# Kernel optimization log

Measured on AMD Instinct MI355X. Metric: run time of the kernel, lower is better.

## Reference

```python
import jax, jax.numpy as jnp
import numpy as np

BLOCK = (4, 4, 4)
NUM_HEADS = 8


def setup_inputs() -> dict:
    key = jax.random.key(0)
    ks = jax.random.split(key, 5)
    C = 128
    return {
        "x": jax.random.normal(ks[0], (2, C, 32, 62, 62), dtype=jnp.float32),
        "qkv_w": jax.random.normal(ks[1], (3 * C, C), dtype=jnp.float32) * 0.02,
        "qkv_b": jax.random.normal(ks[2], (3 * C,), dtype=jnp.float32) * 0.02,
        "conv_w": jax.random.normal(ks[3], (C, C, 1, 1, 1), dtype=jnp.float32) * 0.02,
        "conv_b": jax.random.normal(ks[4], (C,), dtype=jnp.float32) * 0.02,
    }


def reference(x, qkv_w, qkv_b, conv_w, conv_b):
    b0, b1, b2 = BLOCK
    heads = NUM_HEADS
    B, C, D, H0, W0 = x.shape
    pad_r = (-W0) % b2
    pad_b = (-H0) % b1
    x = jnp.pad(x, ((0, 0), (0, 0), (0, 0), (0, pad_b), (0, pad_r)))
    H, W = H0 + pad_b, W0 + pad_r
    d, h, w = D // b0, H // b1, W // b2
    hd = C // heads
    scale = hd ** (-0.5)
    T = b0 * b1 * b2  # tokens per 3D window
    nw = d * h * w    # number of windows

    # partition into windows: (B, nw, T, C)
    xw = x.reshape(B, C, d, b0, h, b1, w, b2).transpose(0, 2, 4, 6, 3, 5, 7, 1)
    xw = xw.reshape(B, nw, T, C)

    qkv = xw @ qkv_w.T + qkv_b  # (B, nw, T, 3C)
    qkv = qkv.reshape(B, nw, T, 3, heads, hd).transpose(3, 0, 1, 4, 2, 5)
    q, k, v = qkv[0], qkv[1], qkv[2]  # (B, nw, heads, T, hd)

    attn = jnp.einsum('bnhtc,bnhsc->bnhts', q, k) * scale

    if pad_r > 0 or pad_b > 0:
        mask = jnp.zeros((H, W), dtype=attn.dtype)
        if pad_b > 0:
            mask = mask.at[-pad_b:, :].set(1.0)
        if pad_r > 0:
            mask = mask.at[:, -pad_r:].set(1.0)
        # (h*w, b1*b2) per-2D-window pad flags
        mask = mask.reshape(h, b1, w, b2).transpose(0, 2, 1, 3).reshape(h * w, b1 * b2)
        am = mask[:, None, :] - mask[:, :, None]  # (h*w, b1*b2, b1*b2)
        am = jnp.where(am != 0, jnp.asarray(-1000.0, attn.dtype), jnp.asarray(0.0, attn.dtype))
        # tile over depth windows and depth tokens (matches torch .repeat)
        am = jnp.tile(am, (d, b0, b0))  # (nw, T, T)
        attn = attn + am[None, :, None, :, :]

    attn = jax.nn.softmax(attn, axis=-1)
    o = jnp.einsum('bnhts,bnhsc->bnhtc', attn, v)  # (B, nw, heads, T, hd)

    o = o.reshape(B, d, h, w, heads, b0, b1, b2, hd)
    o = o.transpose(0, 4, 8, 1, 5, 2, 6, 3, 7).reshape(B, C, D, H, W)
    o = o[:, :, :, :H0, :W0]

    # 1x1x1 Conv3d == channel mixing
    out = jnp.einsum('bcdhw,oc->bodhw', o, conv_w[:, :, 0, 0, 0])
    out = out + conv_b[None, :, None, None, None]
    return out
```

## Files before the change

### kernel.cpp

```cpp
#include <hip/hip_runtime.h>

typedef _Float16 f16x8 __attribute__((ext_vector_type(8)));
typedef _Float16 f16x4 __attribute__((ext_vector_type(4)));
typedef __fp16   fp16x2 __attribute__((ext_vector_type(2)));
typedef float    f32x4 __attribute__((ext_vector_type(4)));
typedef unsigned int u32x2 __attribute__((ext_vector_type(2)));

__device__ __forceinline__ f32x4 mfma32(f16x8 a, f16x8 b, f32x4 c) {
  return __builtin_amdgcn_mfma_f32_16x16x32_f16(a, b, c, 0, 0, 0);
}
__device__ __forceinline__ f32x4 mfma16(f16x4 a, f16x4 b, f32x4 c) {
#if __has_builtin(__builtin_amdgcn_mfma_f32_16x16x16f16)
  return __builtin_amdgcn_mfma_f32_16x16x16f16(a, b, c, 0, 0, 0);
#else
  f32x4 d;
  asm volatile("v_mfma_f32_16x16x16_f16 %0, %1, %2, %3"
               : "=v"(d) : "v"(a), "v"(b), "v"(c));
  return d;
#endif
}

__device__ __forceinline__ unsigned pk2(float a, float b) {
  union { fp16x2 h; unsigned u; } cv;
  cv.h = __builtin_amdgcn_cvt_pkrtz(a, b);
  return cv.u;
}

#define TR_READ(dst, addr, OFF) \
  asm volatile("ds_read_b64_tr_b16 %0, %1 offset:" OFF \
               : "=v"(dst) : "v"(addr) : "memory")

__global__ void cvt_weights(const float* __restrict__ qw, const float* __restrict__ cw,
                            _Float16* __restrict__ wq, _Float16* __restrict__ wc) {
  const int i = blockIdx.x * 256 + threadIdx.x;
  if (i < 384 * 128) wq[i] = (_Float16)qw[i];
  if (i < 128 * 128) wc[i] = (_Float16)cw[i];
}

__global__ void __launch_bounds__(256, 4)
win_attn(const float* __restrict__ xg, const _Float16* __restrict__ wq,
         const float* __restrict__ qbias, const _Float16* __restrict__ wc,
         const float* __restrict__ cb, float* __restrict__ outg)
{
  __shared__ char xsm[16384];
  __shared__ char wsm[4][6144];

  const int tid  = threadIdx.x;
  const int lane = tid & 63;
  const int wv   = tid >> 6;
  const int l15  = lane & 15;
  const int g    = lane >> 4;

  const int raw = blockIdx.x;
  const int wid = ((raw & 7) << 9) | (raw >> 3);
  const int ww = wid & 15, hh = (wid >> 4) & 15, dd = (wid >> 8) & 7, bb = wid >> 11;

  const f32x4 fz = {0.f, 0.f, 0.f, 0.f};

  {
    const int m4 = lane & 3, q4 = lane >> 2;
    const int i0 = q4 >> 2, i1 = q4 & 3;
    const int z = dd * 4 + i0, y = hh * 4 + i1;
    const bool yv   = (y < 62);
    const bool full = (ww < 15);
    float va[8][4];
#pragma unroll
    for (int it = 0; it < 8; ++it) {
      const int c = wv * 32 + it * 4 + m4;
      const float* src = xg + (((size_t)(bb * 128 + c) * 32 + (size_t)z) * 3844
                               + (size_t)(y * 62 + ww * 4));
      float a0 = 0.f, a1 = 0.f, a2 = 0.f, a3 = 0.f;
      if (yv) {
        const float2 lo = *reinterpret_cast<const float2*>(src);
        a0 = lo.x; a1 = lo.y;
        if (full) {
          const float2 hi = *reinterpret_cast<const float2*>(src + 2);
          a2 = hi.x; a3 = hi.y;
        }
      }
      va[it][0] = a0; va[it][1] = a1; va[it][2] = a2; va[it][3] = a3;
    }
#pragma unroll
    for (int it = 0; it < 8; ++it) {
      float v0 = va[it][0], v1 = va[it][1], v2 = va[it][2], v3 = va[it][3];
      float t0 = __shfl_xor((m4 & 1) ? v0 : v1, 1);
      float t1 = __shfl_xor((m4 & 1) ? v2 : v3, 1);
      if (m4 & 1) { v0 = t0; v2 = t1; } else { v1 = t0; v3 = t1; }
      float t2 = __shfl_xor((m4 & 2) ? v0 : v2, 2);
      float t3 = __shfl_xor((m4 & 2) ? v1 : v3, 2);
      if (m4 & 2) { v0 = t2; v1 = t3; } else { v2 = t2; v3 = t3; }
      f16x4 pk; pk[0] = (_Float16)v0; pk[1] = (_Float16)v1;
                pk[2] = (_Float16)v2; pk[3] = (_Float16)v3;
      const int c0 = wv * 32 + it * 4;
      *reinterpret_cast<f16x4*>(xsm + ((lane * 256 + 2 * c0) ^ ((lane & 15) << 4))) = pk;
    }
  }
  __syncthreads();

  char* sb = wsm[wv];
  const unsigned sb32 = (unsigned)(unsigned long long)sb;
  const unsigned trb  = sb32 + 8u * (unsigned)lane;
  const int vswz = (l15 & 7) << 4;

  unsigned long long pm = 0ull;
  if (hh == 15) pm |= 0xFF00FF00FF00FF00ull;
  if (ww == 15) pm |= 0xCCCCCCCCCCCCCCCCull;

  const float LOG2E = 1.4426950408889634f;
  const int swzA = l15 << 4;

  unsigned opk0[4][2], opk1[4][2];

#pragma unroll
  for (int hp = 0; hp < 2; ++hp) {
    __builtin_amdgcn_sched_barrier(0);
#pragma unroll
    for (int co = 0; co < 3; ++co) {
      f32x4 acc[4] = {fz, fz, fz, fz};
      const int col = co * 128 + wv * 32 + hp * 16 + l15;
#pragma unroll
      for (int kk = 0; kk < 4; ++kk) {
        const f16x8 bfr = *reinterpret_cast<const f16x8*>(wq + col * 128 + kk * 32 + g * 8);
#pragma unroll
        for (int ri = 0; ri < 4; ++ri) {
          const f16x8 a = *reinterpret_cast<const f16x8*>(
              xsm + (ri * 16 + l15) * 256 + ((kk * 64 + g * 16) ^ swzA));
          acc[ri] = mfma32(a, bfr, acc[ri]);
        }
      }
      const float bias = qbias[col];
      const float sc = (co == 0) ? 0.25f : 1.0f;
#pragma unroll
      for (int ri = 0; ri < 4; ++ri)
#pragma unroll
        for (int r = 0; r < 4; ++r) acc[ri][r] = (acc[ri][r] + bias) * sc;

      if (co == 2) {
#pragma unroll
        for (int ri = 0; ri < 4; ++ri) {
          const int s0 = ri * 16 + g * 4;
          *reinterpret_cast<unsigned*>(sb + 4096 + l15 * 128 + ((2 * s0) ^ vswz))
              = pk2(acc[ri][0], acc[ri][1]);
          *reinterpret_cast<unsigned*>(sb + 4096 + l15 * 128 + ((2 * (s0 + 2)) ^ vswz))
              = pk2(acc[ri][2], acc[ri][3]);
        }
      } else {
        const int base = (co == 0) ? 2048 : 0;
#pragma unroll
        for (int ri = 0; ri < 4; ++ri) {
          const int off = ri * 512 + l15 * 32 + g * 8;
          u32x2 w;
          w[0] = pk2(acc[ri][0], acc[ri][1]);
          w[1] = pk2(acc[ri][2], acc[ri][3]);
          *reinterpret_cast<u32x2*>(sb + base + off) = w;
        }
      }
      __builtin_amdgcn_sched_barrier(0);
    }
    asm volatile("s_waitcnt lgkmcnt(0)" ::: "memory");

    f16x4 ka[4], qa[4];
    TR_READ(ka[0], trb, "0");
    TR_READ(ka[1], trb, "512");
    TR_READ(ka[2], trb, "1024");
    TR_READ(ka[3], trb, "1536");
    TR_READ(qa[0], trb, "2048");
    TR_READ(qa[1], trb, "2560");
    TR_READ(qa[2], trb, "3072");
    TR_READ(qa[3], trb, "3584");
    f16x8 av0, av1;
    av0 = *reinterpret_cast<const f16x8*>(sb + 4096 + l15 * 128 + ((g * 16) ^ vswz));
    av1 = *reinterpret_cast<const f16x8*>(sb + 4096 + l15 * 128 + ((64 + g * 16) ^ vswz));
    asm volatile("s_waitcnt lgkmcnt(0)" ::: "memory");
    __builtin_amdgcn_sched_barrier(0);

    f32x4 oa0, oa1;
#pragma unroll
    for (int tjp = 0; tjp < 2; ++tjp) {
      const int tj0 = 2 * tjp, tj1 = 2 * tjp + 1;
      f32x4 st2[4][2];
#pragma unroll
      for (int si = 0; si < 4; ++si) {
        st2[si][0] = mfma16(ka[si], qa[tj0], fz);
        st2[si][1] = mfma16(ka[si], qa[tj1], fz);
      }

      if (pm) {
#pragma unroll
        for (int tjc = 0; tjc < 2; ++tjc) {
          const int t = (2 * tjp + tjc) * 16 + l15;
          const unsigned ft = (unsigned)(pm >> t) & 1u;
#pragma unroll
          for (int si = 0; si < 4; ++si)
#pragma unroll
            for (int r = 0; r < 4; ++r) {
              const int s = si * 16 + g * 4 + r;
              const unsigned fs = (unsigned)(pm >> s) & 1u;
              if (fs != ft) st2[si][tjc][r] -= 1000.f;
            }
        }
      }

#pragma unroll
      for (int tjc = 0; tjc < 2; ++tjc) {
        float mx = st2[0][tjc][0];
#pragma unroll
        for (int si = 0; si < 4; ++si)
#pragma unroll
          for (int r = 0; r < 4; ++r) mx = fmaxf(mx, st2[si][tjc][r]);
        mx = fmaxf(mx, __shfl_xor(mx, 16));
        mx = fmaxf(mx, __shfl_xor(mx, 32));
        float sum = 0.f;
#pragma unroll
        for (int si = 0; si < 4; ++si)
#pragma unroll
          for (int r = 0; r < 4; ++r) {
            const float e = __builtin_amdgcn_exp2f((st2[si][tjc][r] - mx) * LOG2E);
            st2[si][tjc][r] = e; sum += e;
          }
        sum += __shfl_xor(sum, 16);
        sum += __shfl_xor(sum, 32);
        const float inv = __builtin_amdgcn_rcpf(sum);
#pragma unroll
        for (int si = 0; si < 4; ++si)
#pragma unroll
          for (int r = 0; r < 4; ++r) st2[si][tjc][r] *= inv;
      }

#pragma unroll
      for (int tjc = 0; tjc < 2; ++tjc) {
        const int tl = tjc * 16 + l15;
#pragma unroll
        for (int si = 0; si < 4; ++si) {
          u32x2 w;
          w[0] = pk2(st2[si][tjc][0], st2[si][tjc][1]);
          w[1] = pk2(st2[si][tjc][2], st2[si][tjc][3]);
          *reinterpret_cast<u32x2*>(sb + tl * 128 + ((si * 32 + g * 8) ^ vswz)) = w;
        }
      }
      asm volatile("s_waitcnt lgkmcnt(0)" ::: "memory");

      oa0 = fz; oa1 = fz;
      {
        const f16x8 pa00 = *reinterpret_cast<const f16x8*>(
            sb + l15 * 128 + ((g * 16) ^ vswz));
        const f16x8 pa10 = *reinterpret_cast<const f16x8*>(
            sb + (16 + l15) * 128 + ((g * 16) ^ vswz));
        oa0 = mfma32(av0, pa00, oa0);
        oa1 = mfma32(av0, pa10, oa1);
        const f16x8 pa01 = *reinterpret_cast<const f16x8*>(
            sb + l15 * 128 + ((64 + g * 16) ^ vswz));
        const f16x8 pa11 = *reinterpret_cast<const f16x8*>(
            sb + (16 + l15) * 128 + ((64 + g * 16) ^ vswz));
        oa0 = mfma32(av1, pa01, oa0);
        oa1 = mfma32(av1, pa11, oa1);
      }

      if (hp == 0) {
        opk0[tj0][0] = pk2(oa0[0], oa0[1]); opk0[tj0][1] = pk2(oa0[2], oa0[3]);
        opk0[tj1][0] = pk2(oa1[0], oa1[1]); opk0[tj1][1] = pk2(oa1[2], oa1[3]);
      } else {
        opk1[tj0][0] = pk2(oa0[0], oa0[1]); opk1[tj0][1] = pk2(oa0[2], oa0[3]);
        opk1[tj1][0] = pk2(oa1[0], oa1[1]); opk1[tj1][1] = pk2(oa1[2], oa1[3]);
      }
      __builtin_amdgcn_sched_barrier(0);
    }
  }
  __syncthreads();

#pragma unroll
  for (int tj = 0; tj < 4; ++tj) {
    const int t = tj * 16 + l15;
    u32x2 w0; w0[0] = opk0[tj][0]; w0[1] = opk0[tj][1];
    *reinterpret_cast<u32x2*>(xsm + t * 256 + (((2 * wv) * 32 + g * 8) ^ ((t & 15) << 4))) = w0;
    u32x2 w1; w1[0] = opk1[tj][0]; w1[1] = opk1[tj][1];
    *reinterpret_cast<u32x2*>(xsm + t * 256 + (((2 * wv + 1) * 32 + g * 8) ^ ((t & 15) << 4))) = w1;
  }
  __syncthreads();

  f32x4 cacc[4][2];
#pragma unroll
  for (int i = 0; i < 4; ++i) { cacc[i][0] = fz; cacc[i][1] = fz; }
#pragma unroll
  for (int kk = 0; kk < 4; ++kk) {
    f16x8 a[4];
#pragma unroll
    for (int ri = 0; ri < 4; ++ri)
      a[ri] = *reinterpret_cast<const f16x8*>(
          xsm + (ri * 16 + l15) * 256 + ((kk * 64 + g * 16) ^ swzA));
#pragma unroll
    for (int co = 0; co < 2; ++co) {
      const int cout = wv * 32 + co * 16 + l15;
      const f16x8 bfr = *reinterpret_cast<const f16x8*>(wc + cout * 128 + kk * 32 + g * 8);
#pragma unroll
      for (int ri = 0; ri < 4; ++ri) cacc[ri][co] = mfma32(a[ri], bfr, cacc[ri][co]);
    }
  }
  const int y = hh * 4 + g;
  if (y < 62) {
#pragma unroll
    for (int co = 0; co < 2; ++co) {
      const int cout = wv * 32 + co * 16 + l15;
      const float bias = cb[cout];
#pragma unroll
      for (int ri = 0; ri < 4; ++ri) {
        const int z = dd * 4 + ri;
        float* dst = outg + (((size_t)(bb * 128 + cout) * 32 + (size_t)z) * 3844
                             + (size_t)(y * 62 + ww * 4));
        float2 lo; lo.x = cacc[ri][co][0] + bias; lo.y = cacc[ri][co][1] + bias;
        *reinterpret_cast<float2*>(dst) = lo;
        if (ww < 15) {
          float2 hi; hi.x = cacc[ri][co][2] + bias; hi.y = cacc[ri][co][3] + bias;
          *reinterpret_cast<float2*>(dst + 2) = hi;
        }
      }
    }
  }
}

extern "C" void kernel_launch(void* const* d_in, const int* in_sizes, int n_in,
                              void* d_out, int out_size, void* d_ws, size_t ws_size,
                              hipStream_t stream) {
  const float* x  = (const float*)d_in[0];
  const float* qw = (const float*)d_in[1];
  const float* qb = (const float*)d_in[2];
  const float* cw = (const float*)d_in[3];
  const float* cb = (const float*)d_in[4];
  float* out = (float*)d_out;

  if (ws_size < (size_t)(384 * 128 + 128 * 128) * sizeof(_Float16)) return;
  _Float16* wq = (_Float16*)d_ws;
  _Float16* wc = wq + 384 * 128;

  cvt_weights<<<192, 256, 0, stream>>>(qw, cw, wq, wc);
  win_attn<<<4096, 256, 0, stream>>>(x, wq, qb, wc, cb, out);
}
```

Before: 165.2 us.

## Split window attention across eight waves, one head per wave

The block grows from 256 to 512 threads so each of the 8 waves handles a single attention head instead of two heads in sequence. The x load, QKV projection, attention and output conv are re-partitioned so each wave owns 16 channels. This adds parallelism inside a block and shortens each wave's serial chain. In exchange it doubles per-block LDS for the per-wave scratch buffers, which may reduce how many blocks fit per CU.

Result: slower. 173.3 us (+4.9%).

```diff
diff --git a/kernel.cpp b/kernel.cpp
--- a/kernel.cpp
+++ b/kernel.cpp
@@ -37,13 +37,13 @@
   if (i < 128 * 128) wc[i] = (_Float16)cw[i];
 }
 
-__global__ void __launch_bounds__(256, 4)
+__global__ void __launch_bounds__(512, 4)
 win_attn(const float* __restrict__ xg, const _Float16* __restrict__ wq,
          const float* __restrict__ qbias, const _Float16* __restrict__ wc,
          const float* __restrict__ cb, float* __restrict__ outg)
 {
   __shared__ char xsm[16384];
-  __shared__ char wsm[4][6144];
+  __shared__ char wsm[8][6144];
 
   const int tid  = threadIdx.x;
   const int lane = tid & 63;
@@ -63,10 +63,10 @@
     const int z = dd * 4 + i0, y = hh * 4 + i1;
     const bool yv   = (y < 62);
     const bool full = (ww < 15);
-    float va[8][4];
-#pragma unroll
-    for (int it = 0; it < 8; ++it) {
-      const int c = wv * 32 + it * 4 + m4;
+    float va[4][4];
+#pragma unroll
+    for (int it = 0; it < 4; ++it) {
+      const int c = wv * 16 + it * 4 + m4;
       const float* src = xg + (((size_t)(bb * 128 + c) * 32 + (size_t)z) * 3844
                                + (size_t)(y * 62 + ww * 4));
       float a0 = 0.f, a1 = 0.f, a2 = 0.f, a3 = 0.f;
@@ -81,7 +81,7 @@
       va[it][0] = a0; va[it][1] = a1; va[it][2] = a2; va[it][3] = a3;
     }
 #pragma unroll
-    for (int it = 0; it < 8; ++it) {
+    for (int it = 0; it < 4; ++it) {
       float v0 = va[it][0], v1 = va[it][1], v2 = va[it][2], v3 = va[it][3];
       float t0 = __shfl_xor((m4 & 1) ? v0 : v1, 1);
       float t1 = __shfl_xor((m4 & 1) ? v2 : v3, 1);
@@ -91,7 +91,7 @@
       if (m4 & 2) { v0 = t2; v1 = t3; } else { v2 = t2; v3 = t3; }
       f16x4 pk; pk[0] = (_Float16)v0; pk[1] = (_Float16)v1;
                 pk[2] = (_Float16)v2; pk[3] = (_Float16)v3;
-      const int c0 = wv * 32 + it * 4;
+      const int c0 = wv * 16 + it * 4;
       *reinterpret_cast<f16x4*>(xsm + ((lane * 256 + 2 * c0) ^ ((lane & 15) << 4))) = pk;
     }
   }
@@ -109,210 +109,191 @@
   const float LOG2E = 1.4426950408889634f;
   const int swzA = l15 << 4;
 
-  unsigned opk0[4][2], opk1[4][2];
-
-#pragma unroll
-  for (int hp = 0; hp < 2; ++hp) {
+#pragma unroll
+  for (int co = 0; co < 3; ++co) {
+    f32x4 acc[4] = {fz, fz, fz, fz};
+    const int col = co * 128 + wv * 16 + l15;
+#pragma unroll
+    for (int kk = 0; kk < 4; ++kk) {
+      const f16x8 bfr = *reinterpret_cast<const f16x8*>(wq + col * 128 + kk * 32 + g * 8);
+#pragma unroll
+      for (int ri = 0; ri < 4; ++ri) {
+        const f16x8 a = *reinterpret_cast<const f16x8*>(
+            xsm + (ri * 16 + l15) * 256 + ((kk * 64 + g * 16) ^ swzA));
+        acc[ri] = mfma32(a, bfr, acc[ri]);
+      }
+    }
+    const float bias = qbias[col];
+    const float sc = (co == 0) ? 0.25f : 1.0f;
+#pragma unroll
+    for (int ri = 0; ri < 4; ++ri)
+#pragma unroll
+      for (int r = 0; r < 4; ++r) acc[ri][r] = (acc[ri][r] + bias) * sc;
+
+    if (co == 2) {
+#pragma unroll
+      for (int ri = 0; ri < 4; ++ri) {
+        const int s0 = ri * 16 + g * 4;
+        *reinterpret_cast<unsigned*>(sb + 4096 + l15 * 128 + ((2 * s0) ^ vswz))
+            = pk2(acc[ri][0], acc[ri][1]);
+        *reinterpret_cast<unsigned*>(sb + 4096 + l15 * 128 + ((2 * (s0 + 2)) ^ vswz))
+            = pk2(acc[ri][2], acc[ri][3]);
+      }
+    } else {
+      const int base = (co == 0) ? 2048 : 0;
+#pragma unroll
+      for (int ri = 0; ri < 4; ++ri) {
+        const int off = ri * 512 + l15 * 32 + g * 8;
+        u32x2 w;
+        w[0] = pk2(acc[ri][0], acc[ri][1]);
+        w[1] = pk2(acc[ri][2], acc[ri][3]);
+        *reinterpret_cast<u32x2*>(sb + base + off) = w;
+      }
+    }
+  }
+  asm volatile("s_waitcnt lgkmcnt(0)" ::: "memory");
+
+  f16x4 ka[4], qa[4];
+  TR_READ(ka[0], trb, "0");
+  TR_READ(ka[1], trb, "512");
+  TR_READ(ka[2], trb, "1024");
+  TR_READ(ka[3], trb, "1536");
+  TR_READ(qa[0], trb, "2048");
+  TR_READ(qa[1], trb, "2560");
+  TR_READ(qa[2], trb, "3072");
+  TR_READ(qa[3], trb, "3584");
+  f16x8 av0, av1;
+  av0 = *reinterpret_cast<const f16x8*>(sb + 4096 + l15 * 128 + ((g * 16) ^ vswz));
+  av1 = *reinterpret_cast<const f16x8*>(sb + 4096 + l15 * 128 + ((64 + g * 16) ^ vswz));
+  asm volatile("s_waitcnt lgkmcnt(0)" ::: "memory");
+  __builtin_amdgcn_sched_barrier(0);
+
+  unsigned opk[4][2];
+#pragma unroll
+  for (int tjp = 0; tjp < 2; ++tjp) {
+    const int tj0 = 2 * tjp, tj1 = 2 * tjp + 1;
+    f32x4 st2[4][2];
+#pragma unroll
+    for (int si = 0; si < 4; ++si) {
+      st2[si][0] = mfma16(ka[si], qa[tj0], fz);
+      st2[si][1] = mfma16(ka[si], qa[tj1], fz);
+    }
+
+    if (pm) {
+#pragma unroll
+      for (int tjc = 0; tjc < 2; ++tjc) {
+        const int t = (2 * tjp + tjc) * 16 + l15;
+        const unsigned ft = (unsigned)(pm >> t) & 1u;
+#pragma unroll
+        for (int si = 0; si < 4; ++si)
+#pragma unroll
+          for (int r = 0; r < 4; ++r) {
+            const int s = si * 16 + g * 4 + r;
+            const unsigned fs = (unsigned)(pm >> s) & 1u;
+            if (fs != ft) st2[si][tjc][r] -= 1000.f;
+          }
+      }
+    }
+
+#pragma unroll
+    for (int tjc = 0; tjc < 2; ++tjc) {
+      float mx = st2[0][tjc][0];
+#pragma unroll
+      for (int si = 0; si < 4; ++si)
+#pragma unroll
+        for (int r = 0; r < 4; ++r) mx = fmaxf(mx, st2[si][tjc][r]);
+      mx = fmaxf(mx, __shfl_xor(mx, 16));
+      mx = fmaxf(mx, __shfl_xor(mx, 32));
+      float sum = 0.f;
+#pragma unroll
+      for (int si = 0; si < 4; ++si)
+#pragma unroll
+        for (int r = 0; r < 4; ++r) {
+          const float e = __builtin_amdgcn_exp2f((st2[si][tjc][r] - mx) * LOG2E);
+          st2[si][tjc][r] = e; sum += e;
+        }
+      sum += __shfl_xor(sum, 16);
+      sum += __shfl_xor(sum, 32);
+      const float inv = __builtin_amdgcn_rcpf(sum);
+#pragma unroll
+      for (int si = 0; si < 4; ++si)
+#pragma unroll
+        for (int r = 0; r < 4; ++r) st2[si][tjc][r] *= inv;
+    }
+
+#pragma unroll
+    for (int tjc = 0; tjc < 2; ++tjc) {
+      const int tl = tjc * 16 + l15;
+#pragma unroll
+      for (int si = 0; si < 4; ++si) {
+        u32x2 w;
+        w[0] = pk2(st2[si][tjc][0], st2[si][tjc][1]);
+        w[1] = pk2(st2[si][tjc][2], st2[si][tjc][3]);
+        *reinterpret_cast<u32x2*>(sb + tl * 128 + ((si * 32 + g * 8) ^ vswz)) = w;
+      }
+    }
+    asm volatile("s_waitcnt lgkmcnt(0)" ::: "memory");
+
+    f32x4 oa0 = fz, oa1 = fz;
+    {
+      const f16x8 pa00 = *reinterpret_cast<const f16x8*>(
+          sb + l15 * 128 + ((g * 16) ^ vswz));
+      const f16x8 pa10 = *reinterpret_cast<const f16x8*>(
+          sb + (16 + l15) * 128 + ((g * 16) ^ vswz));
+      oa0 = mfma32(av0, pa00, oa0);
+      oa1 = mfma32(av0, pa10, oa1);
+      const f16x8 pa01 = *reinterpret_cast<const f16x8*>(
+          sb + l15 * 128 + ((64 + g * 16) ^ vswz));
+      const f16x8 pa11 = *reinterpret_cast<const f16x8*>(
+          sb + (16 + l15) * 128 + ((64 + g * 16) ^ vswz));
+      oa0 = mfma32(av1, pa01, oa0);
+      oa1 = mfma32(av1, pa11, oa1);
+    }
+
+    if (tjp == 0) {
+      opk[0][0] = pk2(oa0[0], oa0[1]); opk[0][1] = pk2(oa0[2], oa0[3]);
+      opk[1][0] = pk2(oa1[0], oa1[1]); opk[1][1] = pk2(oa1[2], oa1[3]);
+    } else {
+      opk[2][0] = pk2(oa0[0], oa0[1]); opk[2][1] = pk2(oa0[2], oa0[3]);
+      opk[3][0] = pk2(oa1[0], oa1[1]); opk[3][1] = pk2(oa1[2], oa1[3]);
+    }
     __builtin_amdgcn_sched_barrier(0);
-#pragma unroll
-    for (int co = 0; co < 3; ++co) {
-      f32x4 acc[4] = {fz, fz, fz, fz};
-      const int col = co * 128 + wv * 32 + hp * 16 + l15;
-#pragma unroll
-      for (int kk = 0; kk < 4; ++kk) {
-        const f16x8 bfr = *reinterpret_cast<const f16x8*>(wq + col * 128 + kk * 32 + g * 8);
-#pragma unroll
-        for (int ri = 0; ri < 4; ++ri) {
-          const f16x8 a = *reinterpret_cast<const f16x8*>(
-              xsm + (ri * 16 + l15) * 256 + ((kk * 64 + g * 16) ^ swzA));
-          acc[ri] = mfma32(a, bfr, acc[ri]);
-        }
-      }
-      const float bias = qbias[col];
-      const float sc = (co == 0) ? 0.25f : 1.0f;
-#pragma unroll
-      for (int ri = 0; ri < 4; ++ri)
-#pragma unroll
-        for (int r = 0; r < 4; ++r) acc[ri][r] = (acc[ri][r] + bias) * sc;
-
-      if (co == 2) {
-#pragma unroll
-        for (int ri = 0; ri < 4; ++ri) {
-          const int s0 = ri * 16 + g * 4;
-          *reinterpret_cast<unsigned*>(sb + 4096 + l15 * 128 + ((2 * s0) ^ vswz))
-              = pk2(acc[ri][0], acc[ri][1]);
-          *reinterpret_cast<unsigned*>(sb + 4096 + l15 * 128 + ((2 * (s0 + 2)) ^ vswz))
-              = pk2(acc[ri][2], acc[ri][3]);
-        }
-      } else {
-        const int base = (co == 0) ? 2048 : 0;
-#pragma unroll
-        for (int ri = 0; ri < 4; ++ri) {
-          const int off = ri * 512 + l15 * 32 + g * 8;
-          u32x2 w;
-          w[0] = pk2(acc[ri][0], acc[ri][1]);
-          w[1] = pk2(acc[ri][2], acc[ri][3]);
-          *reinterpret_cast<u32x2*>(sb + base + off) = w;
-        }
-      }
-      __builtin_amdgcn_sched_barrier(0);
-    }
-    asm volatile("s_waitcnt lgkmcnt(0)" ::: "memory");
-
-    f16x4 ka[4], qa[4];
-    TR_READ(ka[0], trb, "0");
-    TR_READ(ka[1], trb, "512");
-    TR_READ(ka[2], trb, "1024");
-    TR_READ(ka[3], trb, "1536");
-    TR_READ(qa[0], trb, "2048");
-    TR_READ(qa[1], trb, "2560");
-    TR_READ(qa[2], trb, "3072");
-    TR_READ(qa[3], trb, "3584");
-    f16x8 av0, av1;
-    av0 = *reinterpret_cast<const f16x8*>(sb + 4096 + l15 * 128 + ((g * 16) ^ vswz));
-    av1 = *reinterpret_cast<const f16x8*>(sb + 4096 + l15 * 128 + ((64 + g * 16) ^ vswz));
-    asm volatile("s_waitcnt lgkmcnt(0)" ::: "memory");
-    __builtin_amdgcn_sched_barrier(0);
-
-    f32x4 oa0, oa1;
-#pragma unroll
-    for (int tjp = 0; tjp < 2; ++tjp) {
-      const int tj0 = 2 * tjp, tj1 = 2 * tjp + 1;
-      f32x4 st2[4][2];
-#pragma unroll
-      for (int si = 0; si < 4; ++si) {
-        st2[si][0] = mfma16(ka[si], qa[tj0], fz);
-        st2[si][1] = mfma16(ka[si], qa[tj1], fz);
-      }
-
-      if (pm) {
-#pragma unroll
-        for (int tjc = 0; tjc < 2; ++tjc) {
-          const int t = (2 * tjp + tjc) * 16 + l15;
-          const unsigned ft = (unsigned)(pm >> t) & 1u;
-#pragma unroll
-          for (int si = 0; si < 4; ++si)
-#pragma unroll
-            for (int r = 0; r < 4; ++r) {
-              const int s = si * 16 + g * 4 + r;
-              const unsigned fs = (unsigned)(pm >> s) & 1u;
-              if (fs != ft) st2[si][tjc][r] -= 1000.f;
-            }
-        }
-      }
-
-#pragma unroll
-      for (int tjc = 0; tjc < 2; ++tjc) {
-        float mx = st2[0][tjc][0];
-#pragma unroll
-        for (int si = 0; si < 4; ++si)
-#pragma unroll
-          for (int r = 0; r < 4; ++r) mx = fmaxf(mx, st2[si][tjc][r]);
-        mx = fmaxf(mx, __shfl_xor(mx, 16));
-        mx = fmaxf(mx, __shfl_xor(mx, 32));
-        float sum = 0.f;
-#pragma unroll
-        for (int si = 0; si < 4; ++si)
-#pragma unroll
-          for (int r = 0; r < 4; ++r) {
-            const float e = __builtin_amdgcn_exp2f((st2[si][tjc][r] - mx) * LOG2E);
-            st2[si][tjc][r] = e; sum += e;
-          }
-        sum += __shfl_xor(sum, 16);
-        sum += __shfl_xor(sum, 32);
-        const float inv = __builtin_amdgcn_rcpf(sum);
-#pragma unroll
-        for (int si = 0; si < 4; ++si)
-#pragma unroll
-          for (int r = 0; r < 4; ++r) st2[si][tjc][r] *= inv;
-      }
-
-#pragma unroll
-      for (int tjc = 0; tjc < 2; ++tjc) {
-        const int tl = tjc * 16 + l15;
-#pragma unroll
-        for (int si = 0; si < 4; ++si) {
-          u32x2 w;
-          w[0] = pk2(st2[si][tjc][0], st2[si][tjc][1]);
-          w[1] = pk2(st2[si][tjc][2], st2[si][tjc][3]);
-          *reinterpret_cast<u32x2*>(sb + tl * 128 + ((si * 32 + g * 8) ^ vswz)) = w;
-        }
-      }
-      asm volatile("s_waitcnt lgkmcnt(0)" ::: "memory");
-
-      oa0 = fz; oa1 = fz;
-      {
-        const f16x8 pa00 = *reinterpret_cast<const f16x8*>(
-            sb + l15 * 128 + ((g * 16) ^ vswz));
-        const f16x8 pa10 = *reinterpret_cast<const f16x8*>(
-            sb + (16 + l15) * 128 + ((g * 16) ^ vswz));
-        oa0 = mfma32(av0, pa00, oa0);
-        oa1 = mfma32(av0, pa10, oa1);
-        const f16x8 pa01 = *reinterpret_cast<const f16x8*>(
-            sb + l15 * 128 + ((64 + g * 16) ^ vswz));
-        const f16x8 pa11 = *reinterpret_cast<const f16x8*>(
-            sb + (16 + l15) * 128 + ((64 + g * 16) ^ vswz));
-        oa0 = mfma32(av1, pa01, oa0);
-        oa1 = mfma32(av1, pa11, oa1);
-      }
-
-      if (hp == 0) {
-        opk0[tj0][0] = pk2(oa0[0], oa0[1]); opk0[tj0][1] = pk2(oa0[2], oa0[3]);
-        opk0[tj1][0] = pk2(oa1[0], oa1[1]); opk0[tj1][1] = pk2(oa1[2], oa1[3]);
-      } else {
-        opk1[tj0][0] = pk2(oa0[0], oa0[1]); opk1[tj0][1] = pk2(oa0[2], oa0[3]);
-        opk1[tj1][0] = pk2(oa1[0], oa1[1]); opk1[tj1][1] = pk2(oa1[2], oa1[3]);
-      }
-      __builtin_amdgcn_sched_barrier(0);
-    }
   }
   __syncthreads();
 
 #pragma unroll
   for (int tj = 0; tj < 4; ++tj) {
     const int t = tj * 16 + l15;
-    u32x2 w0; w0[0] = opk0[tj][0]; w0[1] = opk0[tj][1];
-    *reinterpret_cast<u32x2*>(xsm + t * 256 + (((2 * wv) * 32 + g * 8) ^ ((t & 15) << 4))) = w0;
-    u32x2 w1; w1[0] = opk1[tj][0]; w1[1] = opk1[tj][1];
-    *reinterpret_cast<u32x2*>(xsm + t * 256 + (((2 * wv + 1) * 32 + g * 8) ^ ((t & 15) << 4))) = w1;
+    u32x2 w0; w0[0] = opk[tj][0]; w0[1] = opk[tj][1];
+    *reinterpret_cast<u32x2*>(xsm + t * 256 + ((wv * 32 + g * 8) ^ ((t & 15) << 4))) = w0;
   }
   __syncthreads();
 
-  f32x4 cacc[4][2];
-#pragma unroll
-  for (int i = 0; i < 4; ++i) { cacc[i][0] = fz; cacc[i][1] = fz; }
+  f32x4 cacc[4] = {fz, fz, fz, fz};
+  const int cout = wv * 16 + l15;
 #pragma unroll
   for (int kk = 0; kk < 4; ++kk) {
-    f16x8 a[4];
-#pragma unroll
-    for (int ri = 0; ri < 4; ++ri)
-      a[ri] = *reinterpret_cast<const f16x8*>(
+    const f16x8 bfr = *reinterpret_cast<const f16x8*>(wc + cout * 128 + kk * 32 + g * 8);
+#pragma unroll
+    for (int ri = 0; ri < 4; ++ri) {
+      const f16x8 a = *reinterpret_cast<const f16x8*>(
           xsm + (ri * 16 + l15) * 256 + ((kk * 64 + g * 16) ^ swzA));
-#pragma unroll
-    for (int co = 0; co < 2; ++co) {
-      const int cout = wv * 32 + co * 16 + l15;
-      const f16x8 bfr = *reinterpret_cast<const f16x8*>(wc + cout * 128 + kk * 32 + g * 8);
-#pragma unroll
-      for (int ri = 0; ri < 4; ++ri) cacc[ri][co] = mfma32(a[ri], bfr, cacc[ri][co]);
+      cacc[ri] = mfma32(a, bfr, cacc[ri]);
     }
   }
   const int y = hh * 4 + g;
   if (y < 62) {
-#pragma unroll
-    for (int co = 0; co < 2; ++co) {
-      const int cout = wv * 32 + co * 16 + l15;
-      const float bias = cb[cout];
-#pragma unroll
-      for (int ri = 0; ri < 4; ++ri) {
-        const int z = dd * 4 + ri;
-        float* dst = outg + (((size_t)(bb * 128 + cout) * 32 + (size_t)z) * 3844
-                             + (size_t)(y * 62 + ww * 4));
-        float2 lo; lo.x = cacc[ri][co][0] + bias; lo.y = cacc[ri][co][1] + bias;
-        *reinterpret_cast<float2*>(dst) = lo;
-        if (ww < 15) {
-          float2 hi; hi.x = cacc[ri][co][2] + bias; hi.y = cacc[ri][co][3] + bias;
-          *reinterpret_cast<float2*>(dst + 2) = hi;
-        }
+    const float bias = cb[cout];
+#pragma unroll
+    for (int ri = 0; ri < 4; ++ri) {
+      const int z = dd * 4 + ri;
+      float* dst = outg + (((size_t)(bb * 128 + cout) * 32 + (size_t)z) * 3844
+                           + (size_t)(y * 62 + ww * 4));
+      float2 lo; lo.x = cacc[ri][0] + bias; lo.y = cacc[ri][1] + bias;
+      *reinterpret_cast<float2*>(dst) = lo;
+      if (ww < 15) {
+        float2 hi; hi.x = cacc[ri][2] + bias; hi.y = cacc[ri][3] + bias;
+        *reinterpret_cast<float2*>(dst + 2) = hi;
       }
     }
   }
@@ -333,5 +314,5 @@
   _Float16* wc = wq + 384 * 128;
 
   cvt_weights<<<192, 256, 0, stream>>>(qw, cw, wq, wc);
-  win_attn<<<4096, 256, 0, stream>>>(x, wq, qb, wc, cb, out);
-}
+  win_attn<<<4096, 512, 0, stream>>>(x, wq, qb, wc, cb, out);
+}
```
